# Kernel optimization log

Measured on AMD Instinct MI355X. Metric: run time of the kernel, lower is better.

## Reference

```python
import jax, jax.numpy as jnp
import numpy as np

H = 1024        # hidden_size
E = 16          # n_routed_experts
K = 4           # num_experts_per_tok (top_k)
I = 512         # moe_intermediate_size
NS = 2          # n_shared_experts
IS = I * NS     # shared-expert intermediate size
N = 2048        # num_tokens
ROUTED_SCALE = 2.5  # routed_scaling_factor


def setup_inputs() -> dict:
    key = jax.random.key(0)
    ks = jax.random.split(key, 6)
    s = 0.02
    return {
        "hidden_states": jax.random.normal(ks[0], (N, H), jnp.float32),
        "gate_w": jax.random.normal(ks[1], (H, E), jnp.float32) * s,
        "w_gate_up": jax.random.normal(ks[2], (E, H, 2 * I), jnp.float32) * s,
        "w_down": jax.random.normal(ks[3], (E, I, H), jnp.float32) * s,
        "shared_gate_up": jax.random.normal(ks[4], (H, 2 * IS), jnp.float32) * s,
        "shared_down": jax.random.normal(ks[5], (IS, H), jnp.float32) * s,
    }


def _moe_forward(x, gate_w, w_gate_up, w_down, shared_gate_up, shared_down):
    n = x.shape[0]
    # --- router: sigmoid scoring + top-k (num_expert_group=topk_group=1) ---
    router_logits = x @ gate_w                      # [N, E]
    scores = jax.nn.sigmoid(router_logits)
    top_vals, top_idx = jax.lax.top_k(scores, K)    # [N, K]
    # renormalize (norm_topk_prob=True)
    top_w = top_vals / jnp.sum(top_vals, axis=-1, keepdims=True)
    # dense combine weights [N, E], zero outside top-k
    w_dense = jnp.zeros((n, E), x.dtype).at[jnp.arange(n)[:, None], top_idx].add(top_w)

    # --- routed experts: SwiGLU per expert, weighted combine ---
    gu = jnp.einsum("nh,ehf->nef", x, w_gate_up)    # [N, E, 2I]
    act = jax.nn.silu(gu[..., :I]) * gu[..., I:]    # SiluAndMul -> [N, E, I]
    routed = jnp.einsum("nei,eih,ne->nh", act, w_down, w_dense)  # [N, H]

    # --- shared experts MLP (WBLMLP) ---
    gus = x @ shared_gate_up                        # [N, 2*IS]
    shared = (jax.nn.silu(gus[:, :IS]) * gus[:, IS:]) @ shared_down  # [N, H]

    return routed * ROUTED_SCALE + shared


def reference(hidden_states, gate_w, w_gate_up, w_down, shared_gate_up, shared_down):
    return _moe_forward(hidden_states, gate_w, w_gate_up, w_down,
                        shared_gate_up, shared_down)
```

## Files before the change

### kernel.cpp

```cpp
#include <hip/hip_runtime.h>
#include <hip/hip_bf16.h>
#include <stdint.h>

#define NTOK 2048
#define HDIM 1024
#define NEXP 16
#define TOPK 4
#define IR   512
#define ISH  1024
#define RSCALE 2.5f

typedef short bf16x4 __attribute__((ext_vector_type(4)));
typedef short bf16x8 __attribute__((ext_vector_type(8)));
typedef float f32x4  __attribute__((ext_vector_type(4)));

static __device__ __forceinline__ unsigned short f2bf(float f){
  union { float fv; uint32_t u; } v; v.fv = f;
  uint32_t r = v.u + 0x7fffu + ((v.u >> 16) & 1u);
  return (unsigned short)(r >> 16);
}
static __device__ __forceinline__ float bf2f(unsigned short s){
  union { uint32_t u; float f; } v; v.u = ((uint32_t)s) << 16;
  return v.f;
}

static __device__ __forceinline__ void gl_lds16(const void* gp, void* lp){
  __builtin_amdgcn_global_load_lds(
      (const __attribute__((address_space(1))) unsigned int*)gp,
      (__attribute__((address_space(3))) unsigned int*)lp, 16, 0, 0);
}

__global__ __launch_bounds__(256) void prep_kernel(
    const float* __restrict__ x, const float* __restrict__ gw,
    float* __restrict__ topkw, int* __restrict__ choice,
    unsigned short* __restrict__ xbf,
    const float* __restrict__ wgu, unsigned short* __restrict__ wgu_t,
    const float* __restrict__ wdn, unsigned short* __restrict__ wdn_t,
    const float* __restrict__ sgu, unsigned short* __restrict__ sgu_t,
    const float* __restrict__ sdn, unsigned short* __restrict__ sdn_t)
{
  __shared__ float tile[64 * 68];
  const int tid = threadIdx.x;
  const int bid = blockIdx.x;

  if (bid < 512){
    const int lane = tid & 63;
    const int t = bid * 4 + (tid >> 6);
    float s[NEXP];
    #pragma unroll
    for (int e = 0; e < NEXP; e++) s[e] = 0.f;
    #pragma unroll
    for (int j = 0; j < 8; j++){
      const int off = 128 * j + lane * 2;
      float2 xv = *(const float2*)(x + (size_t)t * HDIM + off);
      ushort2 xs = { f2bf(xv.x), f2bf(xv.y) };
      *(ushort2*)(xbf + (size_t)t * HDIM + off) = xs;
      const float4* g0 = (const float4*)(gw + (size_t)off * NEXP);
      const float4* g1 = (const float4*)(gw + (size_t)(off + 1) * NEXP);
      #pragma unroll
      for (int q = 0; q < 4; q++){
        float4 a = g0[q], b = g1[q];
        s[q * 4 + 0] += xv.x * a.x + xv.y * b.x;
        s[q * 4 + 1] += xv.x * a.y + xv.y * b.y;
        s[q * 4 + 2] += xv.x * a.z + xv.y * b.z;
        s[q * 4 + 3] += xv.x * a.w + xv.y * b.w;
      }
    }
    #pragma unroll
    for (int e = 0; e < NEXP; e++){
      #pragma unroll
      for (int off = 32; off; off >>= 1)
        s[e] += __shfl_xor(s[e], off);
    }
    float sc[NEXP];
    #pragma unroll
    for (int e = 0; e < NEXP; e++) sc[e] = 1.f / (1.f + __expf(-s[e]));
    unsigned mask = 0; float w[TOPK]; int id[TOPK];
    #pragma unroll
    for (int k = 0; k < TOPK; k++){
      float best = -1e30f; int bi = 0;
      #pragma unroll
      for (int e = 0; e < NEXP; e++){
        if (!((mask >> e) & 1u) && sc[e] > best){ best = sc[e]; bi = e; }
      }
      mask |= 1u << bi; id[k] = bi; w[k] = best;
    }
    float inv = 1.f / (w[0] + w[1] + w[2] + w[3]);
    if (lane == 0){
      #pragma unroll
      for (int k = 0; k < TOPK; k++){
        topkw[t * TOPK + k] = w[k] * inv;
        choice[t * TOPK + k] = id[k];
      }
    }
    return;
  }

  int id = bid - 512;
  const float* s; unsigned short* d; int R, C, rt, ct;
  if (id < 4096){
    int e = id >> 8, r = id & 255; rt = r >> 4; ct = r & 15;
    R = 1024; C = 1024; s = wgu + (size_t)e * 1048576; d = wgu_t + (size_t)e * 1048576;
  } else if (id < 6144){
    id -= 4096; int e = id >> 7, r = id & 127; rt = r >> 4; ct = r & 15;
    R = 512; C = 1024; s = wdn + (size_t)e * 524288; d = wdn_t + (size_t)e * 524288;
  } else if (id < 6656){
    id -= 6144; rt = id >> 5; ct = id & 31;
    R = 1024; C = 2048; s = sgu; d = sgu_t;
  } else {
    id -= 6656; rt = id >> 4; ct = id & 15;
    R = 1024; C = 1024; s = sdn; d = sdn_t;
  }
  const int r0 = rt * 64, c0 = ct * 64;
  #pragma unroll
  for (int i = 0; i < 4; i++){
    int r = i * 16 + (tid >> 4);
    int c = (tid & 15) * 4;
    float4 v = *(const float4*)(s + (size_t)(r0 + r) * C + c0 + c);
    *(float4*)(tile + r * 68 + c) = v;
  }
  __syncthreads();
  #pragma unroll
  for (int i = 0; i < 4; i++){
    int c = i * 16 + (tid >> 4);
    int r = (tid & 15) * 4;
    bf16x4 pk = { (short)f2bf(tile[(r    ) * 68 + c]), (short)f2bf(tile[(r + 1) * 68 + c]),
                  (short)f2bf(tile[(r + 2) * 68 + c]), (short)f2bf(tile[(r + 3) * 68 + c]) };
    *(bf16x4*)(d + (size_t)(c0 + c) * R + r0 + r) = pk;
  }
}

__global__ __launch_bounds__(256) void build_lists(
    const int* __restrict__ choice, int* __restrict__ counts, int* __restrict__ lists)
{
  const int e = blockIdx.x;
  const int tid = threadIdx.x;
  __shared__ int scnt[256];
  const int base = tid * 32;
  unsigned m = 0; int local = 0;
  #pragma unroll
  for (int i = 0; i < 32; i++){
    bool hit = (choice[base + i] == e);
    m |= (unsigned)hit << i;
    local += hit;
  }
  scnt[tid] = local;
  __syncthreads();
  int v = local;
  for (int off = 1; off < 256; off <<= 1){
    int add = (tid >= off) ? scnt[tid - off] : 0;
    __syncthreads();
    v += add; scnt[tid] = v;
    __syncthreads();
  }
  int pos = v - local;
  #pragma unroll
  for (int i = 0; i < 32; i++){
    if ((m >> i) & 1u) lists[e * NTOK + pos++] = base + i;
  }
  if (tid == 255) counts[e] = v;
}

__global__ __launch_bounds__(256) void gu_gemm(
    const unsigned short* __restrict__ xbf, const unsigned short* __restrict__ wgu_t,
    const unsigned short* __restrict__ sgu_t,
    unsigned short* __restrict__ act_r, unsigned short* __restrict__ act_s,
    const int* __restrict__ lists, const int* __restrict__ counts)
{
  __shared__ unsigned short sA[128 * 32];
  __shared__ unsigned short sB[128 * 32];
  __shared__ int sAid[128];

  const int tid = threadIdx.x;
  const int L = blockIdx.x;
  const bool routed = (L < 512);
  int e, mIdx, n0, count, NPAIR, NCH;
  const unsigned short* Bt;
  unsigned short* act;
  if (routed){
    e = L >> 5; int r = L & 31; mIdx = r & 3; n0 = (r >> 2) * 64;
    count = counts[e]; NPAIR = IR; NCH = 4;
    Bt = wgu_t + (size_t)e * (2 * IR) * HDIM;
    act = act_r;
  } else {
    int v = L - 512;
    e = 0; mIdx = v & 15; n0 = (v >> 4) * 64;
    count = NTOK; NPAIR = ISH; NCH = 16;
    Bt = sgu_t; act = act_s;
  }

  const int wv = tid >> 6, lane = tid & 63, lr = lane & 15, g = lane >> 4;
  const int wm = wv >> 1, wn = wv & 1;

  const unsigned short* bsrc[2];
  #pragma unroll
  for (int it = 0; it < 2; it++){
    int q = tid + it * 256;
    int c = q >> 2, ko = (q & 3) * 8;
    int grp = c >> 5, within = c & 31;
    int grow = n0 + (grp >> 1) * 32 + within + ((grp & 1) ? NPAIR : 0);
    bsrc[it] = Bt + (size_t)grow * HDIM + ko;
  }

  for (int mt = mIdx; mt * 128 < count; mt += NCH){
    const int m0 = mt * 128;
    __syncthreads();
    if (tid < 128){
      int idx = m0 + tid;
      int aid;
      if (routed) aid = (idx < count) ? lists[e * NTOK + idx] : lists[e * NTOK];
      else        aid = idx;
      sAid[tid] = aid;
    }
    __syncthreads();
    const unsigned short* asrc[2];
    #pragma unroll
    for (int it = 0; it < 2; it++){
      int q = tid + it * 256;
      int r = q >> 2, ko = (q & 3) * 8;
      int aid = sAid[r];
      int tok = routed ? (aid >> 2) : aid;
      asrc[it] = xbf + (size_t)tok * HDIM + ko;
    }

    const f32x4 z4 = {0.f, 0.f, 0.f, 0.f};
    f32x4 acc[4][4];
    #pragma unroll
    for (int i = 0; i < 4; i++)
      #pragma unroll
      for (int j = 0; j < 4; j++) acc[i][j] = z4;

    for (int k0 = 0; k0 < HDIM; k0 += 32){
      #pragma unroll
      for (int it = 0; it < 2; it++){
        gl_lds16(asrc[it] + k0, sA + (tid + it * 256) * 8);
        gl_lds16(bsrc[it] + k0, sB + (tid + it * 256) * 8);
      }
      __syncthreads();
      bf16x8 af[4], bfr[4];
      #pragma unroll
      for (int i = 0; i < 4; i++){
        af[i]  = *(const bf16x8*)(sA + (wm * 64 + i * 16 + lr) * 32 + g * 8);
        bfr[i] = *(const bf16x8*)(sB + (wn * 64 + i * 16 + lr) * 32 + g * 8);
      }
      #pragma unroll
      for (int mi = 0; mi < 4; mi++)
        #pragma unroll
        for (int ni = 0; ni < 4; ni++)
          acc[mi][ni] = __builtin_amdgcn_mfma_f32_16x16x32_bf16(af[mi], bfr[ni], acc[mi][ni], 0, 0, 0);
      __syncthreads();
    }

    #pragma unroll
    for (int mi = 0; mi < 4; mi++){
      #pragma unroll
      for (int r = 0; r < 4; r++){
        int row = wm * 64 + mi * 16 + g * 4 + r;
        if (routed && m0 + row >= count) continue;
        int aid = sAid[row];
        size_t arow = (size_t)aid * NPAIR;
        #pragma unroll
        for (int ni = 0; ni < 2; ni++){
          float gv = acc[mi][ni][r];
          float uv = acc[mi][ni + 2][r];
          float a = gv / (1.f + __expf(-gv)) * uv;
          act[arow + n0 + wn * 32 + ni * 16 + lr] = f2bf(a);
        }
      }
    }
  }
}

__global__ __launch_bounds__(256) void down_gemm(
    const unsigned short* __restrict__ act_r, const unsigned short* __restrict__ act_s,
    const unsigned short* __restrict__ wdn_t, const unsigned short* __restrict__ sdn_t,
    float* __restrict__ out, unsigned short* __restrict__ downout,
    const int* __restrict__ lists, const int* __restrict__ counts)
{
  __shared__ unsigned short sA[128 * 32];
  __shared__ unsigned short sB[128 * 32];
  __shared__ int sAid[128];

  const int tid = threadIdx.x;
  const int L = blockIdx.x;
  const bool routed = (L < 512);
  int e, mIdx, n0, count, K, NCH;
  const unsigned short* Bt;
  const unsigned short* Ab;
  if (routed){
    e = L >> 5; int r = L & 31; mIdx = r & 3; n0 = (r >> 2) * 128;
    count = counts[e]; K = IR; NCH = 4;
    Bt = wdn_t + (size_t)e * HDIM * IR;
    Ab = act_r;
  } else {
    int v = L - 512;
    e = 0; mIdx = v & 15; n0 = (v >> 4) * 128;
    count = NTOK; K = ISH; NCH = 16;
    Bt = sdn_t; Ab = act_s;
  }

  const int wv = tid >> 6, lane = tid & 63, lr = lane & 15, g = lane >> 4;
  const int wm = wv >> 1, wn = wv & 1;

  const unsigned short* bsrc[2];
  #pragma unroll
  for (int it = 0; it < 2; it++){
    int q = tid + it * 256;
    int c = q >> 2, ko = (q & 3) * 8;
    bsrc[it] = Bt + (size_t)(n0 + c) * K + ko;
  }

  for (int mt = mIdx; mt * 128 < count; mt += NCH){
    const int m0 = mt * 128;
    __syncthreads();
    if (tid < 128){
      int idx = m0 + tid;
      int aid;
      if (routed) aid = (idx < count) ? lists[e * NTOK + idx] : lists[e * NTOK];
      else        aid = idx;
      sAid[tid] = aid;
    }
    __syncthreads();
    const unsigned short* asrc[2];
    #pragma unroll
    for (int it = 0; it < 2; it++){
      int q = tid + it * 256;
      int r = q >> 2, ko = (q & 3) * 8;
      asrc[it] = Ab + (size_t)sAid[r] * K + ko;
    }

    const f32x4 z4 = {0.f, 0.f, 0.f, 0.f};
    f32x4 acc[4][4];
    #pragma unroll
    for (int i = 0; i < 4; i++)
      #pragma unroll
      for (int j = 0; j < 4; j++) acc[i][j] = z4;

    for (int k0 = 0; k0 < K; k0 += 32){
      #pragma unroll
      for (int it = 0; it < 2; it++){
        gl_lds16(asrc[it] + k0, sA + (tid + it * 256) * 8);
        gl_lds16(bsrc[it] + k0, sB + (tid + it * 256) * 8);
      }
      __syncthreads();
      bf16x8 af[4], bfr[4];
      #pragma unroll
      for (int i = 0; i < 4; i++){
        af[i]  = *(const bf16x8*)(sA + (wm * 64 + i * 16 + lr) * 32 + g * 8);
        bfr[i] = *(const bf16x8*)(sB + (wn * 64 + i * 16 + lr) * 32 + g * 8);
      }
      #pragma unroll
      for (int mi = 0; mi < 4; mi++)
        #pragma unroll
        for (int ni = 0; ni < 4; ni++)
          acc[mi][ni] = __builtin_amdgcn_mfma_f32_16x16x32_bf16(af[mi], bfr[ni], acc[mi][ni], 0, 0, 0);
      __syncthreads();
    }

    #pragma unroll
    for (int mi = 0; mi < 4; mi++){
      #pragma unroll
      for (int r = 0; r < 4; r++){
        int row = wm * 64 + mi * 16 + g * 4 + r;
        if (m0 + row >= count) continue;
        int aid = sAid[row];
        size_t orow = (size_t)aid * HDIM;
        if (routed){
          #pragma unroll
          for (int ni = 0; ni < 4; ni++)
            downout[orow + n0 + wn * 64 + ni * 16 + lr] = f2bf(acc[mi][ni][r]);
        } else {
          #pragma unroll
          for (int ni = 0; ni < 4; ni++)
            out[orow + n0 + wn * 64 + ni * 16 + lr] = acc[mi][ni][r];
        }
      }
    }
  }
}

__global__ __launch_bounds__(256) void combine_kernel(
    float* __restrict__ out, const unsigned short* __restrict__ downout,
    const float* __restrict__ topkw)
{
  const int idx = blockIdx.x * 256 + threadIdx.x;
  const int t = idx >> 8;
  const int c4 = (idx & 255) * 4;
  float4 o = *(float4*)(out + (size_t)t * HDIM + c4);
  float r0 = 0.f, r1 = 0.f, r2 = 0.f, r3 = 0.f;
  #pragma unroll
  for (int k = 0; k < TOPK; k++){
    float w = topkw[t * TOPK + k];
    const ushort4 dv = *(const ushort4*)(downout + (size_t)(t * TOPK + k) * HDIM + c4);
    r0 += w * bf2f(dv.x); r1 += w * bf2f(dv.y);
    r2 += w * bf2f(dv.z); r3 += w * bf2f(dv.w);
  }
  o.x += RSCALE * r0; o.y += RSCALE * r1; o.z += RSCALE * r2; o.w += RSCALE * r3;
  *(float4*)(out + (size_t)t * HDIM + c4) = o;
}

extern "C" void kernel_launch(void* const* d_in, const int* in_sizes, int n_in,
                              void* d_out, int out_size, void* d_ws, size_t ws_size,
                              hipStream_t stream) {
  const float* x   = (const float*)d_in[0];
  const float* gw  = (const float*)d_in[1];
  const float* wgu = (const float*)d_in[2];
  const float* wdn = (const float*)d_in[3];
  const float* sgu = (const float*)d_in[4];
  const float* sdn = (const float*)d_in[5];
  float* out = (float*)d_out;

  char* ws = (char*)d_ws;
  float* topkw = (float*)(ws + 0);
  int* choice  = (int*)(ws + 32768);
  int* counts  = (int*)(ws + 65536);
  int* lists   = (int*)(ws + 65792);
  unsigned short* xbf   = (unsigned short*)(ws + 197120);
  unsigned short* wgu_t = (unsigned short*)(ws + 197120 + 4194304ull);
  unsigned short* wdn_t = (unsigned short*)(ws + 197120 + 37748736ull);
  unsigned short* sgu_t = (unsigned short*)(ws + 197120 + 54525952ull);
  unsigned short* sdn_t = (unsigned short*)(ws + 197120 + 58720256ull);
  unsigned short* act_r = (unsigned short*)(ws + 197120 + 60817408ull);
  unsigned short* act_s = (unsigned short*)(ws + 197120 + 69206016ull);
  unsigned short* downout = wgu_t;

  prep_kernel<<<512 + 6912, 256, 0, stream>>>(x, gw, topkw, choice, xbf,
                                              wgu, wgu_t, wdn, wdn_t,
                                              sgu, sgu_t, sdn, sdn_t);
  build_lists<<<NEXP, 256, 0, stream>>>(choice, counts, lists);
  gu_gemm<<<768, 256, 0, stream>>>(xbf, wgu_t, sgu_t, act_r, act_s, lists, counts);
  down_gemm<<<640, 256, 0, stream>>>(act_r, act_s, wdn_t, sdn_t, out, downout, lists, counts);
  combine_kernel<<<(NTOK * HDIM / 4) / 256, 256, 0, stream>>>(out, downout, topkw);
}
```

Before: 140.4 us.

## Widen GEMM K-step, remap block indices, and vectorize transpose writes

```diff
diff --git a/kernel.cpp b/kernel.cpp
--- a/kernel.cpp
+++ b/kernel.cpp
@@ -22,6 +22,11 @@
 static __device__ __forceinline__ float bf2f(unsigned short s){
   union { uint32_t u; float f; } v; v.u = ((uint32_t)s) << 16;
   return v.f;
+}
+static __device__ __forceinline__ unsigned int pkbf2(float lo, float hi){
+  union { __hip_bfloat162 b; unsigned int u; } cv;
+  cv.b = __float22bfloat162_rn(make_float2(lo, hi));
+  return cv.u;
 }
 
 static __device__ __forceinline__ void gl_lds16(const void* gp, void* lp){
@@ -39,7 +44,7 @@
     const float* __restrict__ sgu, unsigned short* __restrict__ sgu_t,
     const float* __restrict__ sdn, unsigned short* __restrict__ sdn_t)
 {
-  __shared__ float tile[64 * 68];
+  __shared__ float tile[64 * 69];
   const int tid = threadIdx.x;
   const int bid = blockIdx.x;
 
@@ -117,16 +122,18 @@
     int r = i * 16 + (tid >> 4);
     int c = (tid & 15) * 4;
     float4 v = *(const float4*)(s + (size_t)(r0 + r) * C + c0 + c);
-    *(float4*)(tile + r * 68 + c) = v;
+    *(float4*)(tile + r * 69 + c) = v;
   }
   __syncthreads();
   #pragma unroll
-  for (int i = 0; i < 4; i++){
-    int c = i * 16 + (tid >> 4);
-    int r = (tid & 15) * 4;
-    bf16x4 pk = { (short)f2bf(tile[(r    ) * 68 + c]), (short)f2bf(tile[(r + 1) * 68 + c]),
-                  (short)f2bf(tile[(r + 2) * 68 + c]), (short)f2bf(tile[(r + 3) * 68 + c]) };
-    *(bf16x4*)(d + (size_t)(c0 + c) * R + r0 + r) = pk;
+  for (int it = 0; it < 2; it++){
+    int q = tid + it * 256;
+    int c = q >> 3, rg = (q & 7) * 8;
+    union { bf16x8 v; unsigned int u[4]; } pk;
+    #pragma unroll
+    for (int k = 0; k < 4; k++)
+      pk.u[k] = pkbf2(tile[(rg + 2 * k) * 69 + c], tile[(rg + 2 * k + 1) * 69 + c]);
+    *(bf16x8*)(d + (size_t)(c0 + c) * R + r0 + rg) = pk.v;
   }
 }
 
@@ -167,8 +174,8 @@
     unsigned short* __restrict__ act_r, unsigned short* __restrict__ act_s,
     const int* __restrict__ lists, const int* __restrict__ counts)
 {
-  __shared__ unsigned short sA[128 * 32];
-  __shared__ unsigned short sB[128 * 32];
+  __shared__ unsigned short sA[2][128 * 32];
+  __shared__ unsigned short sB[2][128 * 32];
   __shared__ int sAid[128];
 
   const int tid = threadIdx.x;
@@ -178,13 +185,14 @@
   const unsigned short* Bt;
   unsigned short* act;
   if (routed){
-    e = L >> 5; int r = L & 31; mIdx = r & 3; n0 = (r >> 2) * 64;
+    int p = L & 7, t = L >> 3;
+    mIdx = t & 3; e = t >> 2; n0 = p * 64;
     count = counts[e]; NPAIR = IR; NCH = 4;
     Bt = wgu_t + (size_t)e * (2 * IR) * HDIM;
     act = act_r;
   } else {
     int v = L - 512;
-    e = 0; mIdx = v & 15; n0 = (v >> 4) * 64;
+    e = 0; n0 = (v & 15) * 64; mIdx = v >> 4;
     count = NTOK; NPAIR = ISH; NCH = 16;
     Bt = sgu_t; act = act_s;
   }
@@ -230,24 +238,29 @@
       #pragma unroll
       for (int j = 0; j < 4; j++) acc[i][j] = z4;
 
-    for (int k0 = 0; k0 < HDIM; k0 += 32){
+    for (int k0 = 0; k0 < HDIM; k0 += 64){
       #pragma unroll
       for (int it = 0; it < 2; it++){
-        gl_lds16(asrc[it] + k0, sA + (tid + it * 256) * 8);
-        gl_lds16(bsrc[it] + k0, sB + (tid + it * 256) * 8);
+        gl_lds16(asrc[it] + k0,      sA[0] + (tid + it * 256) * 8);
+        gl_lds16(asrc[it] + k0 + 32, sA[1] + (tid + it * 256) * 8);
+        gl_lds16(bsrc[it] + k0,      sB[0] + (tid + it * 256) * 8);
+        gl_lds16(bsrc[it] + k0 + 32, sB[1] + (tid + it * 256) * 8);
       }
       __syncthreads();
-      bf16x8 af[4], bfr[4];
-      #pragma unroll
-      for (int i = 0; i < 4; i++){
-        af[i]  = *(const bf16x8*)(sA + (wm * 64 + i * 16 + lr) * 32 + g * 8);
-        bfr[i] = *(const bf16x8*)(sB + (wn * 64 + i * 16 + lr) * 32 + g * 8);
-      }
-      #pragma unroll
-      for (int mi = 0; mi < 4; mi++)
+      #pragma unroll
+      for (int h = 0; h < 2; h++){
+        bf16x8 af[4], bfr[4];
         #pragma unroll
-        for (int ni = 0; ni < 4; ni++)
-          acc[mi][ni] = __builtin_amdgcn_mfma_f32_16x16x32_bf16(af[mi], bfr[ni], acc[mi][ni], 0, 0, 0);
+        for (int i = 0; i < 4; i++){
+          af[i]  = *(const bf16x8*)(sA[h] + (wm * 64 + i * 16 + lr) * 32 + g * 8);
+          bfr[i] = *(const bf16x8*)(sB[h] + (wn * 64 + i * 16 + lr) * 32 + g * 8);
+        }
+        #pragma unroll
+        for (int mi = 0; mi < 4; mi++)
+          #pragma unroll
+          for (int ni = 0; ni < 4; ni++)
+            acc[mi][ni] = __builtin_amdgcn_mfma_f32_16x16x32_bf16(af[mi], bfr[ni], acc[mi][ni], 0, 0, 0);
+      }
       __syncthreads();
     }
 
@@ -277,8 +290,8 @@
     float* __restrict__ out, unsigned short* __restrict__ downout,
     const int* __restrict__ lists, const int* __restrict__ counts)
 {
-  __shared__ unsigned short sA[128 * 32];
-  __shared__ unsigned short sB[128 * 32];
+  __shared__ unsigned short sA[2][128 * 32];
+  __shared__ unsigned short sB[2][128 * 32];
   __shared__ int sAid[128];
 
   const int tid = threadIdx.x;
@@ -288,13 +301,14 @@
   const unsigned short* Bt;
   const unsigned short* Ab;
   if (routed){
-    e = L >> 5; int r = L & 31; mIdx = r & 3; n0 = (r >> 2) * 128;
+    int p = L & 7, t = L >> 3;
+    mIdx = t & 3; e = t >> 2; n0 = p * 128;
     count = counts[e]; K = IR; NCH = 4;
     Bt = wdn_t + (size_t)e * HDIM * IR;
     Ab = act_r;
   } else {
     int v = L - 512;
-    e = 0; mIdx = v & 15; n0 = (v >> 4) * 128;
+    e = 0; n0 = (v & 7) * 128; mIdx = v >> 3;
     count = NTOK; K = ISH; NCH = 16;
     Bt = sdn_t; Ab = act_s;
   }
@@ -336,24 +350,29 @@
       #pragma unroll
       for (int j = 0; j < 4; j++) acc[i][j] = z4;
 
-    for (int k0 = 0; k0 < K; k0 += 32){
+    for (int k0 = 0; k0 < K; k0 += 64){
       #pragma unroll
       for (int it = 0; it < 2; it++){
-        gl_lds16(asrc[it] + k0, sA + (tid + it * 256) * 8);
-        gl_lds16(bsrc[it] + k0, sB + (tid + it * 256) * 8);
+        gl_lds16(asrc[it] + k0,      sA[0] + (tid + it * 256) * 8);
+        gl_lds16(asrc[it] + k0 + 32, sA[1] + (tid + it * 256) * 8);
+        gl_lds16(bsrc[it] + k0,      sB[0] + (tid + it * 256) * 8);
+        gl_lds16(bsrc[it] + k0 + 32, sB[1] + (tid + it * 256) * 8);
       }
       __syncthreads();
-      bf16x8 af[4], bfr[4];
-      #pragma unroll
-      for (int i = 0; i < 4; i++){
-        af[i]  = *(const bf16x8*)(sA + (wm * 64 + i * 16 + lr) * 32 + g * 8);
-        bfr[i] = *(const bf16x8*)(sB + (wn * 64 + i * 16 + lr) * 32 + g * 8);
-      }
-      #pragma unroll
-      for (int mi = 0; mi < 4; mi++)
+      #pragma unroll
+      for (int h = 0; h < 2; h++){
+        bf16x8 af[4], bfr[4];
         #pragma unroll
-        for (int ni = 0; ni < 4; ni++)
-          acc[mi][ni] = __builtin_amdgcn_mfma_f32_16x16x32_bf16(af[mi], bfr[ni], acc[mi][ni], 0, 0, 0);
+        for (int i = 0; i < 4; i++){
+          af[i]  = *(const bf16x8*)(sA[h] + (wm * 64 + i * 16 + lr) * 32 + g * 8);
+          bfr[i] = *(const bf16x8*)(sB[h] + (wn * 64 + i * 16 + lr) * 32 + g * 8);
+        }
+        #pragma unroll
+        for (int mi = 0; mi < 4; mi++)
+          #pragma unroll
+          for (int ni = 0; ni < 4; ni++)
+            acc[mi][ni] = __builtin_amdgcn_mfma_f32_16x16x32_bf16(af[mi], bfr[ni], acc[mi][ni], 0, 0, 0);
+      }
       __syncthreads();
     }
 
```

Measured after the change: 132.6 us. -5.6%, faster.
